# Kernel optimization log

Hardware: AMD Instinct MI355X
Metric: run time of the kernel (lower is better)

Reference implementation:

```python
import jax, jax.numpy as jnp
import numpy as np

DEPTH = 2
DIM = 512
HEADS = 8
DH = 64
INNER = HEADS * DH
MLP = 2048
B = 2
N = 2048
EPS = 1e-6
NEG = -float(np.finfo(np.float32).max)
SCALE = DH ** -0.5


def setup_inputs() -> dict:
    key = jax.random.key(0)
    ks = jax.random.split(key, 8)
    inp = {
        'x': jax.random.normal(ks[0], (B, N, DIM), dtype=jnp.float32),
        'mask': jax.random.randint(ks[1], (B, N), 0, 2, dtype=jnp.int32),
        'qkv_w': 0.02 * jax.random.normal(ks[2], (DEPTH, DIM, 3 * INNER), dtype=jnp.float32),
        'out_w': 0.02 * jax.random.normal(ks[3], (DEPTH, INNER, DIM), dtype=jnp.float32),
        'out_b': jnp.zeros((DEPTH, DIM), dtype=jnp.float32),
        'ff_w1': 0.02 * jax.random.normal(ks[4], (DEPTH, DIM, MLP), dtype=jnp.float32),
        'ff_b1': jnp.zeros((DEPTH, MLP), dtype=jnp.float32),
        'ff_w2': 0.02 * jax.random.normal(ks[5], (DEPTH, MLP, DIM), dtype=jnp.float32),
        'ff_b2': jnp.zeros((DEPTH, DIM), dtype=jnp.float32),
        'ad1_w': jnp.ones((DEPTH, B * DIM), dtype=jnp.float32),
        'ad1_b': jnp.zeros((DEPTH, B * DIM), dtype=jnp.float32),
        'ad2_w': jnp.ones((DEPTH, B * DIM), dtype=jnp.float32),
        'ad2_b': jnp.zeros((DEPTH, B * DIM), dtype=jnp.float32),
    }
    return inp


def adain(x, w, b):
    # AdaptiveInstanceNorm2d: batch_norm over channels (B*D), spatial dim N, training=True
    # -> per-(b, d) mean/biased-var over N, affine params of shape (B*D,) -> (B,1,D)
    mu = jnp.mean(x, axis=1, keepdims=True)
    var = jnp.var(x, axis=1, keepdims=True)  # biased variance, as in batch_norm
    xn = (x - mu) * jax.lax.rsqrt(var + EPS)
    b_sz, _, d = x.shape
    return xn * w.reshape(b_sz, 1, d) + b.reshape(b_sz, 1, d)


def attention(x, mask2d, qkv_w, out_w, out_b):
    b_sz, n, _ = x.shape
    qkv = x @ qkv_w  # [B,N,3*INNER]
    q, k, v = jnp.split(qkv, 3, axis=-1)

    def split_heads(t):
        return t.reshape(b_sz, n, HEADS, DH).transpose(0, 2, 1, 3)  # [B,H,N,D]

    q, k, v = split_heads(q), split_heads(k), split_heads(v)
    dots = jnp.einsum('bhnd,bhmd->bhnm', q, k) * SCALE  # [B,H,N,N]
    dots = jnp.where(mask2d[:, None] == 0, NEG, dots)
    attn = jax.nn.softmax(dots, axis=-1)
    out = jnp.einsum('bhnm,bhmd->bhnd', attn, v)
    out = out.transpose(0, 2, 1, 3).reshape(b_sz, n, INNER)
    return out @ out_w + out_b


def feedforward(x, w1, b1, w2, b2):
    h = jax.nn.gelu(x @ w1 + b1, approximate=False)  # torch nn.GELU default = exact erf
    return h @ w2 + b2


def reference(x, mask, qkv_w, out_w, out_b, ff_w1, ff_b1, ff_w2, ff_b2,
              ad1_w, ad1_b, ad2_w, ad2_b):
    mask2d = mask[:, :, None] * mask[:, None, :]  # [B,N,N]
    for l in range(DEPTH):
        h = adain(x, ad1_w[l], ad1_b[l])
        x = attention(h, mask2d, qkv_w[l], out_w[l], out_b[l]) + x
        h = adain(x, ad2_w[l], ad2_b[l])
        x = feedforward(h, ff_w1[l], ff_b1[l], ff_w2[l], ff_b2[l]) + x
    return x
```

## Files before the change

kernel.cpp:

```cpp
#include <hip/hip_runtime.h>
#include <hip/hip_bf16.h>

#define DEPTHL 2
#define DIMM   512
#define NHEADS 8
#define DHH    64
#define INNERD 512
#define MLPD   2048
#define BB     2
#define SEQL   2048
#define ROWS   (BB*SEQL)
#define MNEG   (-1.0e38f)
#define SCLQ   0.18033688f
#define NSPLIT 4
#define KPS    (SEQL / NSPLIT)
#define NCH    128

typedef __attribute__((ext_vector_type(4))) float f32x4;
typedef __attribute__((ext_vector_type(8))) __bf16 bf16x8;

#define GLDS16(g, l) __builtin_amdgcn_global_load_lds((const __attribute__((address_space(1))) void*)(g), (__attribute__((address_space(3))) void*)(l), 16, 0, 0)

__device__ __forceinline__ unsigned short f2bf(float f) {
  union { float f; unsigned int u; } v; v.f = f;
  unsigned int r = v.u + 0x7fffu + ((v.u >> 16) & 1u);
  return (unsigned short)(r >> 16);
}
__device__ __forceinline__ float bf2f(unsigned short h) {
  union { unsigned int u; float f; } v; v.u = ((unsigned int)h) << 16; return v.f;
}
__device__ __forceinline__ unsigned int cvtpk(float a, float b) {
  unsigned int r;
  asm("v_cvt_pk_bf16_f32 %0, %1, %2" : "=v"(r) : "v"(a), "v"(b));
  return r;
}

__global__ __launch_bounds__(256) void wtrans(const float* __restrict__ wsrc,
                                              unsigned short* __restrict__ wdst,
                                              int K, int N) {
  __shared__ float t[32][33];
  const float* src = wsrc + (size_t)blockIdx.z * K * N;
  unsigned short* dst = wdst + (size_t)blockIdx.z * K * N;
  int k0 = blockIdx.x * 32, n0 = blockIdx.y * 32;
  int tx = threadIdx.x & 31, ty = threadIdx.x >> 5;
#pragma unroll
  for (int j = 0; j < 32; j += 8)
    t[ty + j][tx] = src[(size_t)(k0 + ty + j) * N + n0 + tx];
  __syncthreads();
#pragma unroll
  for (int j = 0; j < 32; j += 8)
    dst[(size_t)(n0 + ty + j) * K + k0 + tx] = f2bf(t[tx][ty + j]);
}

__global__ __launch_bounds__(512) void adain_p1(const float* __restrict__ x,
                                                float* __restrict__ p1, float* __restrict__ p2) {
  int d = threadIdx.x, c = blockIdx.x, b = blockIdx.y;
  const float* xp = x + ((size_t)b * SEQL + c * 16) * DIMM + d;
  float s = 0.f, s2 = 0.f;
#pragma unroll
  for (int i = 0; i < 16; ++i) { float v = xp[(size_t)i * DIMM]; s += v; s2 += v * v; }
  p1[(b * NCH + c) * DIMM + d] = s;
  p2[(b * NCH + c) * DIMM + d] = s2;
}

__global__ __launch_bounds__(512) void adain_p2(const float* __restrict__ p1, const float* __restrict__ p2,
                                                const float* __restrict__ w, const float* __restrict__ bi,
                                                float* __restrict__ alpha, float* __restrict__ beta) {
  int d = threadIdx.x, b = blockIdx.x;
  float s = 0.f, s2 = 0.f;
  for (int c = 0; c < NCH; ++c) { s += p1[(b * NCH + c) * DIMM + d]; s2 += p2[(b * NCH + c) * DIMM + d]; }
  float mean = s * (1.0f / SEQL);
  float var = s2 * (1.0f / SEQL) - mean * mean;
  float a = w[b * DIMM + d] * rsqrtf(var + 1e-6f);
  alpha[b * DIMM + d] = a;
  beta[b * DIMM + d] = bi[b * DIMM + d] - mean * a;
}

__global__ __launch_bounds__(256) void adain_apply(const float* __restrict__ x,
                                                   const float* __restrict__ alpha, const float* __restrict__ beta,
                                                   unsigned short* __restrict__ hb) {
  int idx = blockIdx.x * 256 + threadIdx.x;
  int d = idx & (DIMM - 1);
  int b = idx >> 20;
  hb[idx] = f2bf(x[idx] * alpha[b * DIMM + d] + beta[b * DIMM + d]);
}

__global__ __launch_bounds__(256) void maskbuild(const int* __restrict__ mask, float* __restrict__ maskadd) {
  int i = blockIdx.x * 256 + threadIdx.x;
  maskadd[i] = mask[i] ? 0.f : MNEG;
}

template <int EPI, int BN>
__global__ __launch_bounds__(256)
void gemm_k(const unsigned short* __restrict__ A,
            const unsigned short* __restrict__ Wt,
            const float* __restrict__ bias,
            const float* __restrict__ resid,
            float* __restrict__ outF,
            unsigned short* __restrict__ outB,
            unsigned short* __restrict__ part,
            int N, int Kt) {
  constexpr int NI = BN / 32;
  __shared__ __align__(16) unsigned short As[2][128 * 32];
  __shared__ __align__(16) unsigned short Bs[2][BN * 32];
  const int tid = threadIdx.x;
  const int w = tid >> 6, lane = tid & 63;

  unsigned int f = blockIdx.y * gridDim.x + blockIdx.x;
  unsigned int grp = f & 7u, idx = f >> 3;
  unsigned int rpx = gridDim.y >> 3;
  unsigned int by = grp * rpx + idx / gridDim.x;
  unsigned int bx = idx % gridDim.x;

  const int bm = by * 128, bn = bx * BN;
  const int wm = (w >> 1) * 64, wn = (w & 1) * (BN / 2);

  const int nsplit = gridDim.z, sp = blockIdx.z;
  const int Kc = Kt / nsplit;
  const int kbeg = sp * Kc, kend = kbeg + Kc;

  f32x4 acc[4][NI] = {};

  auto stage = [&](int buf, int k0) {
#pragma unroll
    for (int j = 0; j < 2; ++j) {
      int r = w * 32 + (lane >> 2) + j * 16;
      int cl = (lane & 3) ^ ((r >> 1) & 3);
      GLDS16(A + (size_t)(bm + r) * Kt + k0 + cl * 8, &As[buf][(w * 32 + j * 16) * 32]);
    }
    if (BN == 128) {
#pragma unroll
      for (int j = 0; j < 2; ++j) {
        int r = w * 32 + (lane >> 2) + j * 16;
        int cl = (lane & 3) ^ ((r >> 1) & 3);
        GLDS16(Wt + (size_t)(bn + r) * Kt + k0 + cl * 8, &Bs[buf][(w * 32 + j * 16) * 32]);
      }
    } else {
      int r = w * 16 + (lane >> 2);
      int cl = (lane & 3) ^ ((r >> 1) & 3);
      GLDS16(Wt + (size_t)(bn + r) * Kt + k0 + cl * 8, &Bs[buf][(w * 16) * 32]);
    }
  };

  stage(0, kbeg);
  __syncthreads();
  int cur = 0;

  for (int k0 = kbeg; k0 < kend; k0 += 32) {
    if (k0 + 32 < kend) stage(cur ^ 1, k0 + 32);
    bf16x8 af[4], bfr[NI];
#pragma unroll
    for (int i = 0; i < 4; ++i) {
      int ar = wm + i * 16 + (lane & 15);
      int ac = (lane >> 4) ^ ((ar >> 1) & 3);
      af[i] = *(const bf16x8*)&As[cur][ar * 32 + ac * 8];
    }
#pragma unroll
    for (int i = 0; i < NI; ++i) {
      int br = wn + i * 16 + (lane & 15);
      int bc = (lane >> 4) ^ ((br >> 1) & 3);
      bfr[i] = *(const bf16x8*)&Bs[cur][br * 32 + bc * 8];
    }
#pragma unroll
    for (int mi = 0; mi < 4; ++mi)
#pragma unroll
      for (int ni = 0; ni < NI; ++ni)
        acc[mi][ni] = __builtin_amdgcn_mfma_f32_16x16x32_bf16(af[mi], bfr[ni], acc[mi][ni], 0, 0, 0);
    __syncthreads();
    cur ^= 1;
  }

  const size_t MN = (size_t)gridDim.y * 128 * N;
#pragma unroll
  for (int mi = 0; mi < 4; ++mi) {
#pragma unroll
    for (int ni = 0; ni < NI; ++ni) {
#pragma unroll
      for (int r = 0; r < 4; ++r) {
        int row = bm + wm + mi * 16 + (lane >> 4) * 4 + r;
        int col = bn + wn + ni * 16 + (lane & 15);
        float v = acc[mi][ni][r];
        size_t o = (size_t)row * N + col;
        if (EPI == 3) {
          part[(size_t)sp * MN + o] = f2bf(v);
        } else {
          if (bias) v += bias[col];
          if (EPI == 1) v = 0.5f * v * (1.0f + erff(v * 0.70710678118f));
          if (EPI == 2) outF[o] = v + resid[o];
          else if (EPI != 2) outB[o] = f2bf(v);
        }
      }
    }
  }
}

template <int NS>
__global__ __launch_bounds__(256) void comb_k(const unsigned short* __restrict__ part,
                                              const float* __restrict__ bias,
                                              const float* __restrict__ resid,
                                              float* __restrict__ outF) {
  size_t idx = ((size_t)blockIdx.x * 256 + threadIdx.x) * 4;
  int col = (int)(idx & 511);
  float a0 = 0.f, a1 = 0.f, a2 = 0.f, a3 = 0.f;
#pragma unroll
  for (int s = 0; s < NS; ++s) {
    uint2 v = *(const uint2*)&part[(size_t)s * ROWS * 512 + idx];
    a0 += bf2f(v.x & 0xffff); a1 += bf2f(v.x >> 16);
    a2 += bf2f(v.y & 0xffff); a3 += bf2f(v.y >> 16);
  }
  f32x4 b = *(const f32x4*)&bias[col];
  f32x4 rs = *(const f32x4*)&resid[idx];
  f32x4 o;
  o[0] = a0 + b[0] + rs[0]; o[1] = a1 + b[1] + rs[1];
  o[2] = a2 + b[2] + rs[2]; o[3] = a3 + b[3] + rs[3];
  *(f32x4*)&outF[idx] = o;
}

__global__ __launch_bounds__(256) void qkv_prep(const unsigned short* __restrict__ qkv,
                                                unsigned short* __restrict__ q,
                                                unsigned short* __restrict__ k,
                                                unsigned short* __restrict__ vt,
                                                float* __restrict__ vsum) {
  __shared__ unsigned short t[64][65];
  const int bh = blockIdx.x, nt = blockIdx.y;
  const int b = bh >> 3, h = bh & 7;
  const int n0 = nt * 64;
  const int tid = threadIdx.x;
  const int nloc = tid >> 3, dh0 = (tid & 7) * 8;
#pragma unroll
  for (int j = 0; j < 2; ++j) {
    int n = nloc + j * 32;
    size_t src = (size_t)(b * SEQL + n0 + n) * 1536 + h * 64 + dh0;
    size_t dst = ((size_t)bh * SEQL + n0 + n) * 64 + dh0;
    uint4 qv = *(const uint4*)&qkv[src];
    uint4 qs;
    qs.x = cvtpk(bf2f(qv.x & 0xffff) * SCLQ, bf2f(qv.x >> 16) * SCLQ);
    qs.y = cvtpk(bf2f(qv.y & 0xffff) * SCLQ, bf2f(qv.y >> 16) * SCLQ);
    qs.z = cvtpk(bf2f(qv.z & 0xffff) * SCLQ, bf2f(qv.z >> 16) * SCLQ);
    qs.w = cvtpk(bf2f(qv.w & 0xffff) * SCLQ, bf2f(qv.w >> 16) * SCLQ);
    *(uint4*)&q[dst] = qs;
    *(uint4*)&k[dst] = *(const uint4*)&qkv[src + INNERD];
    uint4 vv = *(const uint4*)&qkv[src + 2 * INNERD];
    unsigned short* tr = &t[n][dh0];
    tr[0] = (unsigned short)(vv.x & 0xffff); tr[1] = (unsigned short)(vv.x >> 16);
    tr[2] = (unsigned short)(vv.y & 0xffff); tr[3] = (unsigned short)(vv.y >> 16);
    tr[4] = (unsigned short)(vv.z & 0xffff); tr[5] = (unsigned short)(vv.z >> 16);
    tr[6] = (unsigned short)(vv.w & 0xffff); tr[7] = (unsigned short)(vv.w >> 16);
  }
  __syncthreads();
#pragma unroll
  for (int j = 0; j < 16; ++j) {
    int i = tid + j * 256;
    int dh = i >> 6, n = i & 63;
    vt[((size_t)bh * DHH + dh) * SEQL + n0 + n] = t[n][dh];
  }
  int dh = tid >> 2, seg = tid & 3;
  float s = 0.f;
#pragma unroll
  for (int i = 0; i < 16; ++i) s += bf2f(t[seg * 16 + i][dh]);
  s += __shfl_xor(s, 1);
  s += __shfl_xor(s, 2);
  if (seg == 0) atomicAdd(&vsum[bh * 64 + dh], s);
}

__global__ __launch_bounds__(256, 4)
void attn_split(const unsigned short* __restrict__ qg,
                const unsigned short* __restrict__ kg,
                const unsigned short* __restrict__ vtg,
                const float* __restrict__ maskadd,
                unsigned short* __restrict__ opart,
                float* __restrict__ lpart) {
  __shared__ __align__(16) unsigned short Ks[2][64 * 64];
  __shared__ __align__(16) unsigned short Vts[2][64 * 64];
  __shared__ __align__(16) unsigned short Ps[4 * 16 * 64];
  const int tid = threadIdx.x, w = tid >> 6, lane = tid & 63;
  const int g = lane >> 4, c = lane & 15;
  const int bh = blockIdx.y, b = bh >> 3;
  const int qt = blockIdx.x;
  const int split = blockIdx.z;
  const int kv0 = split * KPS;
  const int q0 = qt * 64 + w * 16;
  const float* maskb = maskadd + b * SEQL;

  bf16x8 qf[2];
#pragma unroll
  for (int kb = 0; kb < 2; ++kb)
    qf[kb] = *(const bf16x8*)&qg[((size_t)bh * SEQL + q0 + c) * DHH + kb * 32 + g * 8];

  const __bf16 one1 = (__bf16)1.0f;
  const bf16x8 ones = {one1, one1, one1, one1, one1, one1, one1, one1};

  f32x4 o[4] = {};
  f32x4 lones = {};
  unsigned short* myP = &Ps[w * 1024];

  auto stageA = [&](int buf, int kt) {
#pragma unroll
    for (int j = 0; j < 2; ++j) {
      int r = w * 16 + j * 8 + (lane >> 3);
      int cl = (lane & 7) ^ (r & 7);
      GLDS16(kg + ((size_t)bh * SEQL + kv0 + kt * 64 + r) * DHH + cl * 8, &Ks[buf][(w * 16 + j * 8) * 64]);
      GLDS16(vtg + ((size_t)bh * DHH + r) * SEQL + kv0 + kt * 64 + cl * 8, &Vts[buf][(w * 16 + j * 8) * 64]);
    }
  };

  stageA(0, 0);
  __syncthreads();
  int cur = 0;

  for (int kt = 0; kt < KPS / 64; ++kt) {
    if (kt + 1 < KPS / 64) stageA(cur ^ 1, kt + 1);

    f32x4 sT[4];
#pragma unroll
    for (int nt = 0; nt < 4; ++nt)
      sT[nt] = *(const f32x4*)&maskb[kv0 + kt * 64 + nt * 16 + g * 4];
#pragma unroll
    for (int nt = 0; nt < 4; ++nt) {
#pragma unroll
      for (int kb = 0; kb < 2; ++kb) {
        int kr = nt * 16 + c;
        int cs = (kb * 4 + g) ^ (kr & 7);
        bf16x8 kf = *(const bf16x8*)&Ks[cur][kr * 64 + cs * 8];
        sT[nt] = __builtin_amdgcn_mfma_f32_16x16x32_bf16(kf, qf[kb], sT[nt], 0, 0, 0);
      }
    }

#pragma unroll
    for (int nt = 0; nt < 4; ++nt) {
      float pv0 = exp2f(sT[nt][0]), pv1 = exp2f(sT[nt][1]);
      float pv2 = exp2f(sT[nt][2]), pv3 = exp2f(sT[nt][3]);
      unsigned int lo = cvtpk(pv0, pv1), hi = cvtpk(pv2, pv3);
      int off = c * 64 + (((nt * 2 + (g >> 1)) ^ (c & 7)) << 3) + ((g & 1) << 2);
      *(uint2*)(myP + off) = make_uint2(lo, hi);
    }

#pragma unroll
    for (int kb = 0; kb < 2; ++kb) {
      bf16x8 pf = *(const bf16x8*)&myP[c * 64 + (((kb * 4 + g) ^ (c & 7)) << 3)];
      lones = __builtin_amdgcn_mfma_f32_16x16x32_bf16(pf, ones, lones, 0, 0, 0);
#pragma unroll
      for (int ni = 0; ni < 4; ++ni) {
        int vr = ni * 16 + c;
        int vc = (kb * 4 + g) ^ (vr & 7);
        bf16x8 vf = *(const bf16x8*)&Vts[cur][vr * 64 + vc * 8];
        o[ni] = __builtin_amdgcn_mfma_f32_16x16x32_bf16(pf, vf, o[ni], 0, 0, 0);
      }
    }
    __syncthreads();
    cur ^= 1;
  }

  const size_t pb = ((size_t)split * 16 + bh) * SEQL;
#pragma unroll
  for (int ni = 0; ni < 4; ++ni)
#pragma unroll
    for (int r = 0; r < 4; ++r)
      opart[(pb + q0 + g * 4 + r) * DHH + ni * 16 + c] = f2bf(o[ni][r]);
  if (c == 0) {
#pragma unroll
    for (int r = 0; r < 4; ++r) lpart[pb + q0 + g * 4 + r] = lones[r];
  }
}

__global__ __launch_bounds__(256) void attn_combine(const unsigned short* __restrict__ opart,
                                                    const float* __restrict__ lpart,
                                                    const float* __restrict__ maskadd,
                                                    const float* __restrict__ vsum,
                                                    unsigned short* __restrict__ ctx) {
  int idx = blockIdx.x * 256 + threadIdx.x;
  int dq = idx & 15;
  int q = (idx >> 4) & (SEQL - 1);
  int bh = idx >> 15;
  int d0 = dq * 4;
  int b = bh >> 3, h = bh & 7;
  float o0 = 0.f, o1 = 0.f, o2 = 0.f, o3 = 0.f, L = 0.f;
#pragma unroll
  for (int s = 0; s < NSPLIT; ++s) {
    size_t base = ((size_t)s * 16 + bh) * SEQL + q;
    L += lpart[base];
    uint2 v = *(const uint2*)&opart[base * DHH + d0];
    o0 += bf2f(v.x & 0xffff); o1 += bf2f(v.x >> 16);
    o2 += bf2f(v.y & 0xffff); o3 += bf2f(v.y >> 16);
  }
  float r = 1.0f / L;
  o0 *= r; o1 *= r; o2 *= r; o3 *= r;
  if (maskadd[b * SEQL + q] != 0.f) {
    f32x4 vm = *(const f32x4*)&vsum[bh * 64 + d0];
    o0 = vm[0] * (1.0f / SEQL); o1 = vm[1] * (1.0f / SEQL);
    o2 = vm[2] * (1.0f / SEQL); o3 = vm[3] * (1.0f / SEQL);
  }
  *(uint2*)&ctx[((size_t)(b * SEQL + q)) * INNERD + h * 64 + d0] =
      make_uint2(cvtpk(o0, o1), cvtpk(o2, o3));
}

extern "C" void kernel_launch(void* const* d_in, const int* in_sizes, int n_in,
                              void* d_out, int out_size, void* d_ws, size_t ws_size,
                              hipStream_t stream) {
  (void)in_sizes; (void)n_in; (void)out_size;
  const float* x_in = (const float*)d_in[0];
  const int* mask = (const int*)d_in[1];
  const float* qkv_w = (const float*)d_in[2];
  const float* out_w = (const float*)d_in[3];
  const float* out_b = (const float*)d_in[4];
  const float* ff_w1 = (const float*)d_in[5];
  const float* ff_b1 = (const float*)d_in[6];
  const float* ff_w2 = (const float*)d_in[7];
  const float* ff_b2 = (const float*)d_in[8];
  const float* ad1w = (const float*)d_in[9];
  const float* ad1b = (const float*)d_in[10];
  const float* ad2w = (const float*)d_in[11];
  const float* ad2b = (const float*)d_in[12];

  char* ws = (char*)d_ws;
  size_t off = 0;
  auto alloc = [&](size_t bytes) {
    char* p = ws + off;
    off = (off + bytes + 255) & ~(size_t)255;
    return p;
  };
  unsigned short* wtQ = (unsigned short*)alloc((size_t)DEPTHL * 1536 * 512 * 2);
  unsigned short* wtO = (unsigned short*)alloc((size_t)DEPTHL * 512 * 512 * 2);
  unsigned short* wtF1 = (unsigned short*)alloc((size_t)DEPTHL * 2048 * 512 * 2);
  unsigned short* wtF2 = (unsigned short*)alloc((size_t)DEPTHL * 512 * 2048 * 2);
  float* xc = (float*)alloc((size_t)ROWS * DIMM * 4);
  unsigned short* hbf = (unsigned short*)alloc((size_t)ROWS * DIMM * 2);
  unsigned short* qkvbf = (unsigned short*)alloc((size_t)ROWS * 1536 * 2);
  char* region2 = alloc((size_t)4 * 16 * SEQL * DHH * 2);
  unsigned short* qb = (unsigned short*)region2;
  unsigned short* kb = qb + (size_t)16 * SEQL * DHH;
  unsigned short* vtb = kb + (size_t)16 * SEQL * DHH;
  unsigned short* ctxb = vtb + (size_t)16 * SEQL * DHH;
  unsigned short* h1bf = (unsigned short*)region2;
  float* p1 = (float*)alloc((size_t)BB * NCH * DIMM * 4);
  float* p2 = (float*)alloc((size_t)BB * NCH * DIMM * 4);
  float* alpha = (float*)alloc((size_t)BB * DIMM * 4);
  float* beta = (float*)alloc((size_t)BB * DIMM * 4);
  float* maskadd = (float*)alloc((size_t)BB * SEQL * 4);
  unsigned short* opart = (unsigned short*)alloc((size_t)NSPLIT * 16 * SEQL * DHH * 2);
  float* lpart = (float*)alloc((size_t)NSPLIT * 16 * SEQL * 4);
  float* vsum = (float*)alloc((size_t)16 * 64 * 4);
  unsigned short* part = (unsigned short*)alloc((size_t)4 * ROWS * 512 * 2);
  const bool fits = off <= ws_size;

  hipMemcpyAsync(xc, x_in, (size_t)ROWS * DIMM * 4, hipMemcpyDeviceToDevice, stream);

  wtrans<<<dim3(512 / 32, 1536 / 32, DEPTHL), 256, 0, stream>>>(qkv_w, wtQ, 512, 1536);
  wtrans<<<dim3(512 / 32, 512 / 32, DEPTHL), 256, 0, stream>>>(out_w, wtO, 512, 512);
  wtrans<<<dim3(512 / 32, 2048 / 32, DEPTHL), 256, 0, stream>>>(ff_w1, wtF1, 512, 2048);
  wtrans<<<dim3(2048 / 32, 512 / 32, DEPTHL), 256, 0, stream>>>(ff_w2, wtF2, 2048, 512);
  maskbuild<<<BB * SEQL / 256, 256, 0, stream>>>(mask, maskadd);

  for (int l = 0; l < DEPTHL; ++l) {
    adain_p1<<<dim3(NCH, BB), 512, 0, stream>>>(xc, p1, p2);
    adain_p2<<<BB, 512, 0, stream>>>(p1, p2, ad1w + l * BB * DIMM, ad1b + l * BB * DIMM, alpha, beta);
    adain_apply<<<8192, 256, 0, stream>>>(xc, alpha, beta, hbf);
    gemm_k<0, 64><<<dim3(1536 / 64, ROWS / 128), 256, 0, stream>>>(
        hbf, wtQ + (size_t)l * 1536 * 512, nullptr, nullptr, nullptr, qkvbf, nullptr, 1536, 512);
    hipMemsetAsync(vsum, 0, 16 * 64 * 4, stream);
    qkv_prep<<<dim3(16, 32), 256, 0, stream>>>(qkvbf, qb, kb, vtb, vsum);
    attn_split<<<dim3(SEQL / 64, 16, NSPLIT), 256, 0, stream>>>(qb, kb, vtb, maskadd, opart, lpart);
    attn_combine<<<16 * SEQL * 16 / 256, 256, 0, stream>>>(opart, lpart, maskadd, vsum, ctxb);
    if (fits) {
      gemm_k<3, 64><<<dim3(512 / 64, ROWS / 128, 2), 256, 0, stream>>>(
          ctxb, wtO + (size_t)l * 512 * 512, nullptr, nullptr, nullptr, nullptr, part, 512, 512);
      comb_k<2><<<ROWS * 512 / 1024, 256, 0, stream>>>(part, out_b + l * DIMM, xc, xc);
    } else {
      gemm_k<2, 64><<<dim3(512 / 64, ROWS / 128), 256, 0, stream>>>(
          ctxb, wtO + (size_t)l * 512 * 512, out_b + l * DIMM, xc, xc, nullptr, nullptr, 512, 512);
    }
    adain_p1<<<dim3(NCH, BB), 512, 0, stream>>>(xc, p1, p2);
    adain_p2<<<BB, 512, 0, stream>>>(p1, p2, ad2w + l * BB * DIMM, ad2b + l * BB * DIMM, alpha, beta);
    adain_apply<<<8192, 256, 0, stream>>>(xc, alpha, beta, hbf);
    gemm_k<1, 64><<<dim3(2048 / 64, ROWS / 128), 256, 0, stream>>>(
        hbf, wtF1 + (size_t)l * 2048 * 512, ff_b1 + l * MLPD, nullptr, nullptr, h1bf, nullptr, 2048, 512);
    float* xout = (l == DEPTHL - 1) ? (float*)d_out : xc;
    if (fits) {
      gemm_k<3, 64><<<dim3(512 / 64, ROWS / 128, 4), 256, 0, stream>>>(
          h1bf, wtF2 + (size_t)l * 512 * 2048, nullptr, nullptr, nullptr, nullptr, part, 512, 2048);
      comb_k<4><<<ROWS * 512 / 1024, 256, 0, stream>>>(part, ff_b2 + l * DIMM, xc, xout);
    } else {
      gemm_k<2, 64><<<dim3(512 / 64, ROWS / 128), 256, 0, stream>>>(
          h1bf, wtF2 + (size_t)l * 512 * 2048, ff_b2 + l * DIMM, xc, xout, nullptr, nullptr, 512, 2048);
    }
  }
}
```

Baseline: 337.2 us.

## Double query rows per attention wave, drop K/V double buffering, coarsen AdaIN partials

Each attention wave now handles 32 query rows instead of 16, so every K/V fragment loaded from shared memory feeds two MFMAs and the grid along the query axis halves. The double-buffered K/V staging is replaced by a single buffer that is loaded and then synchronised before compute, which gives up overlap between global loads and math in exchange for less LDS per block. AdaIN partial reduction moves from 128 chunks of 16 rows to 32 chunks of 64 rows, cutting the second-pass work but reducing parallelism in the first pass. More registers per thread may lower occupancy.

Measured after the change: 312.6 us. -7.3%, faster.

```diff
diff --git a/kernel.cpp b/kernel.cpp
--- a/kernel.cpp
+++ b/kernel.cpp
@@ -14,7 +14,6 @@
 #define SCLQ   0.18033688f
 #define NSPLIT 4
 #define KPS    (SEQL / NSPLIT)
-#define NCH    128
 
 typedef __attribute__((ext_vector_type(4))) float f32x4;
 typedef __attribute__((ext_vector_type(8))) __bf16 bf16x8;
@@ -55,12 +54,11 @@
 __global__ __launch_bounds__(512) void adain_p1(const float* __restrict__ x,
                                                 float* __restrict__ p1, float* __restrict__ p2) {
   int d = threadIdx.x, c = blockIdx.x, b = blockIdx.y;
-  const float* xp = x + ((size_t)b * SEQL + c * 16) * DIMM + d;
+  const float* xp = x + ((size_t)b * SEQL + c * 64) * DIMM + d;
   float s = 0.f, s2 = 0.f;
-#pragma unroll
-  for (int i = 0; i < 16; ++i) { float v = xp[(size_t)i * DIMM]; s += v; s2 += v * v; }
-  p1[(b * NCH + c) * DIMM + d] = s;
-  p2[(b * NCH + c) * DIMM + d] = s2;
+  for (int i = 0; i < 64; ++i) { float v = xp[(size_t)i * DIMM]; s += v; s2 += v * v; }
+  p1[(b * 32 + c) * DIMM + d] = s;
+  p2[(b * 32 + c) * DIMM + d] = s2;
 }
 
 __global__ __launch_bounds__(512) void adain_p2(const float* __restrict__ p1, const float* __restrict__ p2,
@@ -68,7 +66,7 @@
                                                 float* __restrict__ alpha, float* __restrict__ beta) {
   int d = threadIdx.x, b = blockIdx.x;
   float s = 0.f, s2 = 0.f;
-  for (int c = 0; c < NCH; ++c) { s += p1[(b * NCH + c) * DIMM + d]; s2 += p2[(b * NCH + c) * DIMM + d]; }
+  for (int c = 0; c < 32; ++c) { s += p1[(b * 32 + c) * DIMM + d]; s2 += p2[(b * 32 + c) * DIMM + d]; }
   float mean = s * (1.0f / SEQL);
   float var = s2 * (1.0f / SEQL) - mean * mean;
   float a = w[b * DIMM + d] * rsqrtf(var + 1e-6f);
@@ -270,96 +268,110 @@
                 const float* __restrict__ maskadd,
                 unsigned short* __restrict__ opart,
                 float* __restrict__ lpart) {
-  __shared__ __align__(16) unsigned short Ks[2][64 * 64];
-  __shared__ __align__(16) unsigned short Vts[2][64 * 64];
-  __shared__ __align__(16) unsigned short Ps[4 * 16 * 64];
+  __shared__ __align__(16) unsigned short Ks[64 * 64];
+  __shared__ __align__(16) unsigned short Vts[64 * 64];
+  __shared__ __align__(16) unsigned short Ps[4 * 32 * 64];
   const int tid = threadIdx.x, w = tid >> 6, lane = tid & 63;
   const int g = lane >> 4, c = lane & 15;
   const int bh = blockIdx.y, b = bh >> 3;
   const int qt = blockIdx.x;
   const int split = blockIdx.z;
   const int kv0 = split * KPS;
-  const int q0 = qt * 64 + w * 16;
+  const int q0 = qt * 128 + w * 32;
   const float* maskb = maskadd + b * SEQL;
 
-  bf16x8 qf[2];
-#pragma unroll
-  for (int kb = 0; kb < 2; ++kb)
-    qf[kb] = *(const bf16x8*)&qg[((size_t)bh * SEQL + q0 + c) * DHH + kb * 32 + g * 8];
+  bf16x8 qf0[2], qf1[2];
+#pragma unroll
+  for (int kb = 0; kb < 2; ++kb) {
+    qf0[kb] = *(const bf16x8*)&qg[((size_t)bh * SEQL + q0 + c) * DHH + kb * 32 + g * 8];
+    qf1[kb] = *(const bf16x8*)&qg[((size_t)bh * SEQL + q0 + 16 + c) * DHH + kb * 32 + g * 8];
+  }
 
   const __bf16 one1 = (__bf16)1.0f;
   const bf16x8 ones = {one1, one1, one1, one1, one1, one1, one1, one1};
 
-  f32x4 o[4] = {};
-  f32x4 lones = {};
-  unsigned short* myP = &Ps[w * 1024];
-
-  auto stageA = [&](int buf, int kt) {
+  f32x4 o0[4] = {}, o1[4] = {};
+  f32x4 lones0 = {}, lones1 = {};
+  unsigned short* myP = &Ps[w * 2048];
+
+  for (int kt = 0; kt < KPS / 64; ++kt) {
 #pragma unroll
     for (int j = 0; j < 2; ++j) {
       int r = w * 16 + j * 8 + (lane >> 3);
       int cl = (lane & 7) ^ (r & 7);
-      GLDS16(kg + ((size_t)bh * SEQL + kv0 + kt * 64 + r) * DHH + cl * 8, &Ks[buf][(w * 16 + j * 8) * 64]);
-      GLDS16(vtg + ((size_t)bh * DHH + r) * SEQL + kv0 + kt * 64 + cl * 8, &Vts[buf][(w * 16 + j * 8) * 64]);
-    }
-  };
-
-  stageA(0, 0);
-  __syncthreads();
-  int cur = 0;
-
-  for (int kt = 0; kt < KPS / 64; ++kt) {
-    if (kt + 1 < KPS / 64) stageA(cur ^ 1, kt + 1);
-
-    f32x4 sT[4];
-#pragma unroll
-    for (int nt = 0; nt < 4; ++nt)
-      sT[nt] = *(const f32x4*)&maskb[kv0 + kt * 64 + nt * 16 + g * 4];
+      GLDS16(kg + ((size_t)bh * SEQL + kv0 + kt * 64 + r) * DHH + cl * 8, &Ks[(w * 16 + j * 8) * 64]);
+      GLDS16(vtg + ((size_t)bh * DHH + r) * SEQL + kv0 + kt * 64 + cl * 8, &Vts[(w * 16 + j * 8) * 64]);
+    }
+    __syncthreads();
+
+    f32x4 sT0[4], sT1[4];
+#pragma unroll
+    for (int nt = 0; nt < 4; ++nt) {
+      f32x4 mk = *(const f32x4*)&maskb[kv0 + kt * 64 + nt * 16 + g * 4];
+      sT0[nt] = mk;
+      sT1[nt] = mk;
+    }
 #pragma unroll
     for (int nt = 0; nt < 4; ++nt) {
 #pragma unroll
       for (int kb = 0; kb < 2; ++kb) {
         int kr = nt * 16 + c;
         int cs = (kb * 4 + g) ^ (kr & 7);
-        bf16x8 kf = *(const bf16x8*)&Ks[cur][kr * 64 + cs * 8];
-        sT[nt] = __builtin_amdgcn_mfma_f32_16x16x32_bf16(kf, qf[kb], sT[nt], 0, 0, 0);
+        bf16x8 kf = *(const bf16x8*)&Ks[kr * 64 + cs * 8];
+        sT0[nt] = __builtin_amdgcn_mfma_f32_16x16x32_bf16(kf, qf0[kb], sT0[nt], 0, 0, 0);
+        sT1[nt] = __builtin_amdgcn_mfma_f32_16x16x32_bf16(kf, qf1[kb], sT1[nt], 0, 0, 0);
       }
     }
 
 #pragma unroll
     for (int nt = 0; nt < 4; ++nt) {
-      float pv0 = exp2f(sT[nt][0]), pv1 = exp2f(sT[nt][1]);
-      float pv2 = exp2f(sT[nt][2]), pv3 = exp2f(sT[nt][3]);
-      unsigned int lo = cvtpk(pv0, pv1), hi = cvtpk(pv2, pv3);
-      int off = c * 64 + (((nt * 2 + (g >> 1)) ^ (c & 7)) << 3) + ((g & 1) << 2);
-      *(uint2*)(myP + off) = make_uint2(lo, hi);
+      int swz = (((nt * 2 + (g >> 1)) ^ (c & 7)) << 3) + ((g & 1) << 2);
+      {
+        float pv0 = exp2f(sT0[nt][0]), pv1 = exp2f(sT0[nt][1]);
+        float pv2 = exp2f(sT0[nt][2]), pv3 = exp2f(sT0[nt][3]);
+        *(uint2*)(myP + c * 64 + swz) = make_uint2(cvtpk(pv0, pv1), cvtpk(pv2, pv3));
+      }
+      {
+        float pv0 = exp2f(sT1[nt][0]), pv1 = exp2f(sT1[nt][1]);
+        float pv2 = exp2f(sT1[nt][2]), pv3 = exp2f(sT1[nt][3]);
+        *(uint2*)(myP + (16 + c) * 64 + swz) = make_uint2(cvtpk(pv0, pv1), cvtpk(pv2, pv3));
+      }
     }
 
 #pragma unroll
     for (int kb = 0; kb < 2; ++kb) {
-      bf16x8 pf = *(const bf16x8*)&myP[c * 64 + (((kb * 4 + g) ^ (c & 7)) << 3)];
-      lones = __builtin_amdgcn_mfma_f32_16x16x32_bf16(pf, ones, lones, 0, 0, 0);
+      int ps = ((kb * 4 + g) ^ (c & 7)) << 3;
+      bf16x8 pf0 = *(const bf16x8*)&myP[c * 64 + ps];
+      bf16x8 pf1 = *(const bf16x8*)&myP[(16 + c) * 64 + ps];
+      lones0 = __builtin_amdgcn_mfma_f32_16x16x32_bf16(pf0, ones, lones0, 0, 0, 0);
+      lones1 = __builtin_amdgcn_mfma_f32_16x16x32_bf16(pf1, ones, lones1, 0, 0, 0);
 #pragma unroll
       for (int ni = 0; ni < 4; ++ni) {
         int vr = ni * 16 + c;
         int vc = (kb * 4 + g) ^ (vr & 7);
-        bf16x8 vf = *(const bf16x8*)&Vts[cur][vr * 64 + vc * 8];
-        o[ni] = __builtin_amdgcn_mfma_f32_16x16x32_bf16(pf, vf, o[ni], 0, 0, 0);
+        bf16x8 vf = *(const bf16x8*)&Vts[vr * 64 + vc * 8];
+        o0[ni] = __builtin_amdgcn_mfma_f32_16x16x32_bf16(pf0, vf, o0[ni], 0, 0, 0);
+        o1[ni] = __builtin_amdgcn_mfma_f32_16x16x32_bf16(pf1, vf, o1[ni], 0, 0, 0);
       }
     }
     __syncthreads();
-    cur ^= 1;
   }
 
   const size_t pb = ((size_t)split * 16 + bh) * SEQL;
 #pragma unroll
-  for (int ni = 0; ni < 4; ++ni)
-#pragma unroll
-    for (int r = 0; r < 4; ++r)
-      opart[(pb + q0 + g * 4 + r) * DHH + ni * 16 + c] = f2bf(o[ni][r]);
+  for (int ni = 0; ni < 4; ++ni) {
+#pragma unroll
+    for (int r = 0; r < 4; ++r) {
+      opart[(pb + q0 + g * 4 + r) * DHH + ni * 16 + c] = f2bf(o0[ni][r]);
+      opart[(pb + q0 + 16 + g * 4 + r) * DHH + ni * 16 + c] = f2bf(o1[ni][r]);
+    }
+  }
   if (c == 0) {
 #pragma unroll
-    for (int r = 0; r < 4; ++r) lpart[pb + q0 + g * 4 + r] = lones[r];
+    for (int r = 0; r < 4; ++r) {
+      lpart[pb + q0 + g * 4 + r] = lones0[r];
+      lpart[pb + q0 + 16 + g * 4 + r] = lones1[r];
+    }
   }
 }
 
@@ -432,8 +444,8 @@
   unsigned short* vtb = kb + (size_t)16 * SEQL * DHH;
   unsigned short* ctxb = vtb + (size_t)16 * SEQL * DHH;
   unsigned short* h1bf = (unsigned short*)region2;
-  float* p1 = (float*)alloc((size_t)BB * NCH * DIMM * 4);
-  float* p2 = (float*)alloc((size_t)BB * NCH * DIMM * 4);
+  float* p1 = (float*)alloc((size_t)BB * 32 * DIMM * 4);
+  float* p2 = (float*)alloc((size_t)BB * 32 * DIMM * 4);
   float* alpha = (float*)alloc((size_t)BB * DIMM * 4);
   float* beta = (float*)alloc((size_t)BB * DIMM * 4);
   float* maskadd = (float*)alloc((size_t)BB * SEQL * 4);
@@ -452,14 +464,14 @@
   maskbuild<<<BB * SEQL / 256, 256, 0, stream>>>(mask, maskadd);
 
   for (int l = 0; l < DEPTHL; ++l) {
-    adain_p1<<<dim3(NCH, BB), 512, 0, stream>>>(xc, p1, p2);
+    adain_p1<<<dim3(32, BB), 512, 0, stream>>>(xc, p1, p2);
     adain_p2<<<BB, 512, 0, stream>>>(p1, p2, ad1w + l * BB * DIMM, ad1b + l * BB * DIMM, alpha, beta);
     adain_apply<<<8192, 256, 0, stream>>>(xc, alpha, beta, hbf);
     gemm_k<0, 64><<<dim3(1536 / 64, ROWS / 128), 256, 0, stream>>>(
         hbf, wtQ + (size_t)l * 1536 * 512, nullptr, nullptr, nullptr, qkvbf, nullptr, 1536, 512);
     hipMemsetAsync(vsum, 0, 16 * 64 * 4, stream);
     qkv_prep<<<dim3(16, 32), 256, 0, stream>>>(qkvbf, qb, kb, vtb, vsum);
-    attn_split<<<dim3(SEQL / 64, 16, NSPLIT), 256, 0, stream>>>(qb, kb, vtb, maskadd, opart, lpart);
+    attn_split<<<dim3(SEQL / 128, 16, NSPLIT), 256, 0, stream>>>(qb, kb, vtb, maskadd, opart, lpart);
     attn_combine<<<16 * SEQL * 16 / 256, 256, 0, stream>>>(opart, lpart, maskadd, vsum, ctxb);
     if (fits) {
       gemm_k<3, 64><<<dim3(512 / 64, ROWS / 128, 2), 256, 0, stream>>>(
@@ -469,7 +481,7 @@
       gemm_k<2, 64><<<dim3(512 / 64, ROWS / 128), 256, 0, stream>>>(
           ctxb, wtO + (size_t)l * 512 * 512, out_b + l * DIMM, xc, xc, nullptr, nullptr, 512, 512);
     }
-    adain_p1<<<dim3(NCH, BB), 512, 0, stream>>>(xc, p1, p2);
+    adain_p1<<<dim3(32, BB), 512, 0, stream>>>(xc, p1, p2);
     adain_p2<<<BB, 512, 0, stream>>>(p1, p2, ad2w + l * BB * DIMM, ad2b + l * BB * DIMM, alpha, beta);
     adain_apply<<<8192, 256, 0, stream>>>(xc, alpha, beta, hbf);
     gemm_k<1, 64><<<dim3(2048 / 64, ROWS / 128), 256, 0, stream>>>(
```
